# Kernel tuning notes

Measured on AMD Instinct MI355X. Metric: run time of the kernel, lower is better.

The kernel has to match this reference:

```python
import jax, jax.numpy as jnp
import numpy as np

B, N, D = 4, 8192, 128
H = 4 * D  # exp_factor * features
EPS = 1e-5


def layer_norm(x):
    # fresh nn.LayerNorm each call -> weight=1, bias=0 (no learned affine)
    mu = jnp.mean(x, axis=-1, keepdims=True)
    var = jnp.var(x, axis=-1, keepdims=True)
    return (x - mu) * jax.lax.rsqrt(var + EPS)


def setup_inputs() -> dict:
    key = jax.random.key(0)
    ks = jax.random.split(key, 8)
    x = jax.random.normal(ks[0], (B, N, D), dtype=jnp.float32)
    adj = jax.random.uniform(ks[1], (N, N), dtype=jnp.float32)
    attn_mask = jnp.ones((1,), dtype=jnp.int32)  # unused (torch masked_fill result discarded)
    pad_mask = jnp.ones((1,), dtype=jnp.int32)   # unused
    # FFN params (torch Linear default init scale ~ 1/sqrt(fan_in))
    w1 = jax.random.normal(ks[2], (D, H), dtype=jnp.float32) / np.sqrt(D)
    b1 = jnp.zeros((H,), dtype=jnp.float32)
    w2 = jax.random.normal(ks[3], (H, D), dtype=jnp.float32) / np.sqrt(H)
    b2 = jnp.zeros((D,), dtype=jnp.float32)
    return {"x": x, "adj": adj, "attn_mask": attn_mask, "pad_mask": pad_mask,
            "w1": w1, "b1": b1, "w2": w2, "b2": b2, "dim": 128}


def reference(x, adj, attn_mask, pad_mask, w1, b1, w2, b2, dim):
    # Sublayer 0: x + InrAwaSA(LN(x))
    h = layer_norm(x)                               # [B,N,D]
    # adj is provided -> scores = dense adj, shared across batch.
    # NOTE: masks are no-ops in the source (masked_fill not in-place).
    prob = jax.nn.softmax(adj, axis=-1)             # [N,N]
    attn_out = jnp.einsum('nm,bmd->bnd', prob, h)   # [B,N,D]
    x1 = x + attn_out
    # Sublayer 1: x1 + FFN(LN(x1))
    h1 = layer_norm(x1)
    ffn = jnp.maximum(h1 @ w1 + b1, 0.0) @ w2 + b2
    return x1 + ffn
```

## Files before the change

kernel.cpp:

```cpp
#include <hip/hip_runtime.h>
#include <hip/hip_bf16.h>

typedef __attribute__((ext_vector_type(8))) short bh8;
typedef __attribute__((ext_vector_type(4))) float fx4;

typedef const __attribute__((address_space(1))) unsigned int* gas_p;
typedef __attribute__((address_space(3))) unsigned int* las_p;

#define MFMA(a, b, c) __builtin_amdgcn_mfma_f32_16x16x32_bf16((a), (b), (c), 0, 0, 0)
#define MFMA8(a, b, c) __builtin_amdgcn_mfma_f32_16x16x32_fp8_fp8((a), (b), (c), 0, 0, 0)

__device__ __forceinline__ unsigned short f2bf(float f) {
  unsigned u = __builtin_bit_cast(unsigned, f);
  u += 0x7fff + ((u >> 16) & 1);
  return (unsigned short)(u >> 16);
}

__device__ __forceinline__ float bflo2f(unsigned u) { return __builtin_bit_cast(float, u << 16); }
__device__ __forceinline__ float bfhi2f(unsigned u) { return __builtin_bit_cast(float, u & 0xffff0000u); }

__device__ __forceinline__ void gld16(const void* g, void* l) {
  __builtin_amdgcn_global_load_lds((gas_p)g, (las_p)l, 16, 0, 0);
}

__global__ __launch_bounds__(256) void transpose_weights(const float* __restrict__ w1,
                                                         const float* __restrict__ w2,
                                                         unsigned short* __restrict__ w1t,
                                                         unsigned short* __restrict__ w2t) {
  const int tgl = blockIdx.x * 256 + threadIdx.x;
  { const int h = tgl >> 7, d = tgl & 127; w1t[tgl] = f2bf(w1[d * 512 + h]); }
  { const int d = tgl >> 9, h = tgl & 511; w2t[tgl] = f2bf(w2[h * 128 + d]); }
}

__global__ __launch_bounds__(256) void ln1_transpose(const float* __restrict__ x,
                                                     unsigned char* __restrict__ ht) {
  const int t = threadIdx.x, lane = t & 63, w = t >> 6;
  const int mt = blockIdx.x, b = blockIdx.y;
  __shared__ unsigned short tile[128 * 64];
  const float* xb = x + ((size_t)b * 8192 + (size_t)mt * 64) * 128;
  for (int it = 0; it < 16; ++it) {
    const int r = w * 16 + it;
    const float2 v = *(const float2*)(xb + r * 128 + lane * 2);
    float s = v.x + v.y, s2 = v.x * v.x + v.y * v.y;
    #pragma unroll
    for (int o = 1; o < 64; o <<= 1) { s += __shfl_xor(s, o); s2 += __shfl_xor(s2, o); }
    const float mean = s * 0.0078125f;
    const float var = s2 * 0.0078125f - mean * mean;
    const float rstd = rsqrtf(var + 1e-5f);
    const int mc = r >> 3, ml = r & 7;
    const int d0 = lane * 2, d1 = d0 + 1;
    tile[d0 * 64 + ((mc ^ (d0 & 7)) << 3) + ml] = f2bf((v.x - mean) * rstd);
    tile[d1 * 64 + ((mc ^ (d1 & 7)) << 3) + ml] = f2bf((v.y - mean) * rstd);
  }
  __syncthreads();
  unsigned char* hb = ht + (size_t)b * 128 * 8192 + (size_t)mt * 64;
  #pragma unroll
  for (int i = 0; i < 4; ++i) {
    const int idx = i * 256 + t;
    const int d = idx >> 3, mc = idx & 7;
    const bh8 vv = *(const bh8*)(tile + d * 64 + ((mc ^ (d & 7)) << 3));
    int lo = 0, hi = 0;
    lo = __builtin_amdgcn_cvt_pk_fp8_f32(bflo2f((unsigned short)vv[0]),
                                         bflo2f((unsigned short)vv[1]), lo, false);
    lo = __builtin_amdgcn_cvt_pk_fp8_f32(bflo2f((unsigned short)vv[2]),
                                         bflo2f((unsigned short)vv[3]), lo, true);
    hi = __builtin_amdgcn_cvt_pk_fp8_f32(bflo2f((unsigned short)vv[4]),
                                         bflo2f((unsigned short)vv[5]), hi, false);
    hi = __builtin_amdgcn_cvt_pk_fp8_f32(bflo2f((unsigned short)vv[6]),
                                         bflo2f((unsigned short)vv[7]), hi, true);
    *(uint2*)(hb + (size_t)d * 8192 + mc * 8) = (uint2){(unsigned)lo, (unsigned)hi};
  }
}

__global__ __launch_bounds__(256) void softmax_rows(const float* __restrict__ adj,
                                                    unsigned char* __restrict__ prob) {
  const int t = threadIdx.x, lane = t & 63, w = t >> 6;
  const size_t r = blockIdx.x;
  __shared__ float red[4];
  const fx4* row = (const fx4*)(adj + r * 8192);
  fx4 v[8];
  float lsum = 0.f;
  #pragma unroll
  for (int i = 0; i < 8; ++i) {
    const fx4 a = row[i * 256 + t];
    fx4 e;
    e.x = __expf(a.x);
    e.y = __expf(a.y);
    e.z = __expf(a.z);
    e.w = __expf(a.w);
    v[i] = e;
    lsum += e.x + e.y + e.z + e.w;
  }
  #pragma unroll
  for (int o = 1; o < 64; o <<= 1) lsum += __shfl_xor(lsum, o);
  if (lane == 0) red[w] = lsum;
  __syncthreads();
  const float rinv = 4096.f / (red[0] + red[1] + red[2] + red[3]);
  unsigned* po = (unsigned*)(prob + r * 8192);
  #pragma unroll
  for (int i = 0; i < 8; ++i) {
    int pk = 0;
    pk = __builtin_amdgcn_cvt_pk_fp8_f32(v[i].x * rinv, v[i].y * rinv, pk, false);
    pk = __builtin_amdgcn_cvt_pk_fp8_f32(v[i].z * rinv, v[i].w * rinv, pk, true);
    po[i * 256 + t] = (unsigned)pk;
  }
}

#define PH_SYNC { __builtin_amdgcn_sched_barrier(0); __builtin_amdgcn_s_barrier(); \
                  __builtin_amdgcn_sched_barrier(0); \
                  asm volatile("s_waitcnt lgkmcnt(0)" ::: "memory"); \
                  __builtin_amdgcn_sched_barrier(0); __builtin_amdgcn_s_setprio(1); }
#define PH_END  { __builtin_amdgcn_s_setprio(0); __builtin_amdgcn_sched_barrier(0); \
                  __builtin_amdgcn_s_barrier(); __builtin_amdgcn_sched_barrier(0); }
#define PH_END_VM2 { __builtin_amdgcn_s_setprio(0); \
                  asm volatile("s_waitcnt vmcnt(2)" ::: "memory"); \
                  __builtin_amdgcn_sched_barrier(0); __builtin_amdgcn_s_barrier(); \
                  __builtin_amdgcn_sched_barrier(0); }

__global__ __launch_bounds__(512, 2) void attn_gemm(const unsigned char* __restrict__ prob,
                                                    const unsigned char* __restrict__ ht,
                                                    unsigned short* __restrict__ pbuf) {
  const int t = threadIdx.x, lane = t & 63, w = t >> 6;
  const int wm = w >> 2, wn = w & 3;
  const int mt = blockIdx.x, nt = blockIdx.y, z = blockIdx.z;
  const int kbase = z * 2048;

  __shared__ unsigned char Al[2][2][128 * 64];
  __shared__ unsigned char Bl[2][2][128 * 64];

  fx4 acc[8][4];
  #pragma unroll
  for (int i = 0; i < 8; ++i)
    #pragma unroll
    for (int j = 0; j < 4; ++j) acc[i][j] = (fx4){0.f, 0.f, 0.f, 0.f};

  long afr[8], bf0[4], bf1[4];

  auto stageA = [&](int buf, int half, int tau) {
    const unsigned char* root = prob + (size_t)(mt * 256 + half * 128) * 8192 + kbase + tau * 64;
    const int r = t >> 2, c = t & 3;
    gld16(root + (size_t)r * 8192 + ((c ^ ((r >> 1) & 3)) << 4), &Al[buf][half][(t & ~63) * 16]);
  };
  auto stageB = [&](int buf, int half, int tau) {
    const unsigned char* root = ht + (size_t)(nt * 256 + half * 128) * 8192 + kbase + tau * 64;
    const int r = t >> 2, c = t & 3;
    gld16(root + (size_t)r * 8192 + ((c ^ ((r >> 1) & 3)) << 4), &Bl[buf][half][(t & ~63) * 16]);
  };
  auto ldA = [&](int buf, int mh) {
    #pragma unroll
    for (int mf = 0; mf < 4; ++mf)
      #pragma unroll
      for (int kk = 0; kk < 2; ++kk) {
        const int r = mh * 64 + mf * 16 + (lane & 15);
        const int sl = lane >> 4;
        const int g = kk * 2 + (sl >> 1), h = sl & 1;
        afr[mf * 2 + kk] =
            *(const long*)&Al[buf][wm][r * 64 + ((g ^ ((r >> 1) & 3)) << 4) + h * 8];
      }
  };
  auto ldB = [&](int buf, int nh, long* dst) {
    #pragma unroll
    for (int nf = 0; nf < 2; ++nf)
      #pragma unroll
      for (int kk = 0; kk < 2; ++kk) {
        const int c = (wn & 1) * 64 + nh * 32 + nf * 16 + (lane & 15);
        const int sl = lane >> 4;
        const int g = kk * 2 + (sl >> 1), h = sl & 1;
        dst[nf * 2 + kk] =
            *(const long*)&Bl[buf][wn >> 1][c * 64 + ((g ^ ((c >> 1) & 3)) << 4) + h * 8];
      }
  };
  auto mmq = [&](int mh, int nh, const long* bfr) {
    #pragma unroll
    for (int mf = 0; mf < 4; ++mf)
      #pragma unroll
      for (int nf = 0; nf < 2; ++nf)
        #pragma unroll
        for (int kk = 0; kk < 2; ++kk)
          acc[mh * 4 + mf][nh * 2 + nf] =
              MFMA8(afr[mf * 2 + kk], bfr[nf * 2 + kk], acc[mh * 4 + mf][nh * 2 + nf]);
  };

  stageA(0, 0, 0); stageA(0, 1, 0); stageB(0, 0, 0); stageB(0, 1, 0);
  stageB(1, 0, 1); stageB(1, 1, 1);
  asm volatile("s_waitcnt vmcnt(2)" ::: "memory");
  __builtin_amdgcn_sched_barrier(0);
  __builtin_amdgcn_s_barrier();
  __builtin_amdgcn_sched_barrier(0);

  for (int i = 0; i < 15; ++i) {
    const int t0 = 2 * i;
    ldA(0, 0); ldB(0, 0, bf0); stageA(1, 0, t0 + 1);
    PH_SYNC; mmq(0, 0, bf0); PH_END;
    ldB(0, 1, bf1); stageA(1, 1, t0 + 1);
    PH_SYNC; mmq(0, 1, bf1); PH_END;
    ldA(0, 1); stageB(0, 0, t0 + 2);
    PH_SYNC; mmq(1, 1, bf1); PH_END;
    stageB(0, 1, t0 + 2);
    PH_SYNC; mmq(1, 0, bf0); PH_END_VM2;
    ldA(1, 0); ldB(1, 0, bf0); stageA(0, 0, t0 + 2);
    PH_SYNC; mmq(0, 0, bf0); PH_END;
    ldB(1, 1, bf1); stageA(0, 1, t0 + 2);
    PH_SYNC; mmq(0, 1, bf1); PH_END;
    ldA(1, 1); stageB(1, 0, t0 + 3);
    PH_SYNC; mmq(1, 1, bf1); PH_END;
    stageB(1, 1, t0 + 3);
    PH_SYNC; mmq(1, 0, bf0); PH_END_VM2;
  }

  stageA(1, 0, 31); stageA(1, 1, 31);
  asm volatile("s_waitcnt vmcnt(0)" ::: "memory");
  __builtin_amdgcn_sched_barrier(0);
  __builtin_amdgcn_s_barrier();
  __builtin_amdgcn_sched_barrier(0);
  ldA(0, 0); ldB(0, 0, bf0); PH_SYNC; mmq(0, 0, bf0); PH_END;
  ldB(0, 1, bf1);            PH_SYNC; mmq(0, 1, bf1); PH_END;
  ldA(0, 1);                 PH_SYNC; mmq(1, 1, bf1); PH_END;
                             PH_SYNC; mmq(1, 0, bf0); PH_END;
  ldA(1, 0); ldB(1, 0, bf0); PH_SYNC; mmq(0, 0, bf0); PH_END;
  ldB(1, 1, bf1);            PH_SYNC; mmq(0, 1, bf1); PH_END;
  ldA(1, 1);                 PH_SYNC; mmq(1, 1, bf1); PH_END;
                             PH_SYNC; mmq(1, 0, bf0); PH_END;

  const float ds = 0.000244140625f;
  unsigned short* po = pbuf + (size_t)z * 8192 * 512;
  const int grow0 = mt * 256 + wm * 128;
  const int gcol0 = nt * 256 + (wn >> 1) * 128 + (wn & 1) * 64;
  #pragma unroll
  for (int mh = 0; mh < 2; ++mh)
    #pragma unroll
    for (int mf = 0; mf < 4; ++mf)
      #pragma unroll
      for (int nh = 0; nh < 2; ++nh)
        #pragma unroll
        for (int nf = 0; nf < 2; ++nf) {
          const int col = gcol0 + nh * 32 + nf * 16 + (lane & 15);
          #pragma unroll
          for (int q = 0; q < 4; ++q) {
            const int row = grow0 + mh * 64 + mf * 16 + (lane >> 4) * 4 + q;
            po[(size_t)row * 512 + col] = f2bf(acc[mh * 4 + mf][nh * 2 + nf][q] * ds);
          }
        }
}

#define SWZ16(ks, r) (((((ks) & 7) ^ ((r) & 7)) | ((ks) & 8)))
__global__ __launch_bounds__(512) void ln_ffn_kernel(const float* __restrict__ x,
                                                     const unsigned short* __restrict__ pbuf,
                                                     const unsigned short* __restrict__ w1t,
                                                     const unsigned short* __restrict__ w2t,
                                                     const float* __restrict__ b1,
                                                     const float* __restrict__ b2,
                                                     float* __restrict__ out) {
  const int t = threadIdx.x, lane = t & 63, w = t >> 6;
  const int wr = w >> 1, wc = w & 1;
  const int row0 = blockIdx.x * 128;
  __shared__ unsigned short As[128 * 128];
  __shared__ unsigned short W1c[128 * 128];
  __shared__ unsigned short W2c[128 * 128];
  __shared__ unsigned short Ts[128 * 128];

  auto stageW1 = [&](int hc) {
    #pragma unroll
    for (int i = 0; i < 4; ++i) {
      const int idx = i * 512 + t;
      const int row = idx >> 4, kc = idx & 15;
      const int kcs = (kc & 8) | ((kc & 7) ^ (row & 7));
      gld16(w1t + (size_t)(hc * 128 + row) * 128 + kcs * 8, W1c + (idx & ~63) * 8);
    }
  };
  auto stageW2 = [&](int hc) {
    #pragma unroll
    for (int i = 0; i < 4; ++i) {
      const int idx = i * 512 + t;
      const int row = idx >> 4, kc = idx & 15;
      const int kcs = (kc & 8) | ((kc & 7) ^ (row & 7));
      gld16(w2t + (size_t)row * 512 + hc * 128 + kcs * 8, W2c + (idx & ~63) * 8);
    }
  };

  stageW1(0); stageW2(0);

  const int r = t >> 2, q = t & 3, c0 = q * 32;
  const int rowg = row0 + r;
  const int bb = rowg >> 13, nn = rowg & 8191;
  float xv[32];
  {
    const float* xp = x + (size_t)rowg * 128 + c0;
    #pragma unroll
    for (int j = 0; j < 8; ++j) {
      const float4 v4 = *(const float4*)(xp + 4 * j);
      xv[4 * j] = v4.x; xv[4 * j + 1] = v4.y; xv[4 * j + 2] = v4.z; xv[4 * j + 3] = v4.w;
    }
    #pragma unroll
    for (int z = 0; z < 4; ++z) {
      const unsigned short* pp = pbuf + ((size_t)z * 8192 + nn) * 512 + bb * 128 + c0;
      #pragma unroll
      for (int j = 0; j < 4; ++j) {
        const bh8 pv = *(const bh8*)(pp + 8 * j);
        #pragma unroll
        for (int e = 0; e < 8; ++e) xv[8 * j + e] += bflo2f((unsigned short)pv[e]);
      }
    }
  }
  float s = 0.f, s2 = 0.f;
  #pragma unroll
  for (int j = 0; j < 32; ++j) { s += xv[j]; s2 += xv[j] * xv[j]; }
  s += __shfl_xor(s, 1); s2 += __shfl_xor(s2, 1);
  s += __shfl_xor(s, 2); s2 += __shfl_xor(s2, 2);
  const float mean = s * 0.0078125f;
  const float var = s2 * 0.0078125f - mean * mean;
  const float rstd = rsqrtf(var + 1e-5f);
  #pragma unroll
  for (int j = 0; j < 4; ++j) {
    const int g = q * 4 + j;
    bh8 pk;
    #pragma unroll
    for (int e = 0; e < 8; ++e) pk[e] = (short)f2bf((xv[8 * j + e] - mean) * rstd);
    *(bh8*)(As + r * 128 + SWZ16(g, r) * 8) = pk;
  }
  __syncthreads();

  fx4 accO[2][4];
  #pragma unroll
  for (int i = 0; i < 2; ++i)
    #pragma unroll
    for (int j = 0; j < 4; ++j) accO[i][j] = (fx4){0.f, 0.f, 0.f, 0.f};

  for (int hc = 0; hc < 4; ++hc) {
    if (hc > 0) stageW2(hc);
    fx4 accT[2][4];
    #pragma unroll
    for (int i = 0; i < 2; ++i)
      #pragma unroll
      for (int j = 0; j < 4; ++j) accT[i][j] = (fx4){0.f, 0.f, 0.f, 0.f};
    #pragma unroll
    for (int kk = 0; kk < 4; ++kk) {
      const int ks = kk * 4 + (lane >> 4);
      bh8 af[2], bfr[4];
      #pragma unroll
      for (int f = 0; f < 2; ++f) {
        const int ra = wr * 32 + f * 16 + (lane & 15);
        af[f] = *(const bh8*)(As + ra * 128 + SWZ16(ks, ra) * 8);
      }
      #pragma unroll
      for (int f = 0; f < 4; ++f) {
        const int rb = wc * 64 + f * 16 + (lane & 15);
        bfr[f] = *(const bh8*)(W1c + rb * 128 + SWZ16(ks, rb) * 8);
      }
      #pragma unroll
      for (int fm = 0; fm < 2; ++fm)
        #pragma unroll
        for (int fn = 0; fn < 4; ++fn) accT[fm][fn] = MFMA(af[fm], bfr[fn], accT[fm][fn]);
    }
    #pragma unroll
    for (int fm = 0; fm < 2; ++fm)
      #pragma unroll
      for (int fn = 0; fn < 4; ++fn) {
        const int col = wc * 64 + fn * 16 + (lane & 15);
        const float bv = b1[hc * 128 + col];
        const int c = col >> 3;
        #pragma unroll
        for (int qq = 0; qq < 4; ++qq) {
          const int row = wr * 32 + fm * 16 + (lane >> 4) * 4 + qq;
          float vv = accT[fm][fn][qq] + bv;
          vv = fmaxf(vv, 0.f);
          Ts[row * 128 + SWZ16(c, row) * 8 + (col & 7)] = f2bf(vv);
        }
      }
    __syncthreads();
    if (hc < 3) {
      stageW1(hc + 1);
    } else {
      float* dst = (r < 64) ? (float*)As + r * 128 + c0 : (float*)W1c + (r - 64) * 128 + c0;
      #pragma unroll
      for (int j = 0; j < 8; ++j)
        *(float4*)(dst + 4 * j) =
            (float4){xv[4 * j], xv[4 * j + 1], xv[4 * j + 2], xv[4 * j + 3]};
    }
    #pragma unroll
    for (int kk = 0; kk < 4; ++kk) {
      const int ks = kk * 4 + (lane >> 4);
      bh8 af[2], bfr[4];
      #pragma unroll
      for (int f = 0; f < 2; ++f) {
        const int ra = wr * 32 + f * 16 + (lane & 15);
        af[f] = *(const bh8*)(Ts + ra * 128 + SWZ16(ks, ra) * 8);
      }
      #pragma unroll
      for (int f = 0; f < 4; ++f) {
        const int rb = wc * 64 + f * 16 + (lane & 15);
        bfr[f] = *(const bh8*)(W2c + rb * 128 + SWZ16(ks, rb) * 8);
      }
      #pragma unroll
      for (int fm = 0; fm < 2; ++fm)
        #pragma unroll
        for (int fn = 0; fn < 4; ++fn) accO[fm][fn] = MFMA(af[fm], bfr[fn], accO[fm][fn]);
    }
    __syncthreads();
  }

  const float* x1a = (const float*)As;
  const float* x1b = (const float*)W1c;
  float* op = out + (size_t)row0 * 128;
  #pragma unroll
  for (int fm = 0; fm < 2; ++fm)
    #pragma unroll
    for (int fn = 0; fn < 4; ++fn) {
      const int col = wc * 64 + fn * 16 + (lane & 15);
      const float bv = b2[col];
      #pragma unroll
      for (int qq = 0; qq < 4; ++qq) {
        const int row = wr * 32 + fm * 16 + (lane >> 4) * 4 + qq;
        const float x1v = (row < 64) ? x1a[row * 128 + col] : x1b[(row - 64) * 128 + col];
        op[row * 128 + col] = x1v + accO[fm][fn][qq] + bv;
      }
    }
}

extern "C" void kernel_launch(void* const* d_in, const int* in_sizes, int n_in,
                              void* d_out, int out_size, void* d_ws, size_t ws_size,
                              hipStream_t stream) {
  const float* x   = (const float*)d_in[0];
  const float* adj = (const float*)d_in[1];
  const float* w1  = (const float*)d_in[4];
  const float* b1  = (const float*)d_in[5];
  const float* w2  = (const float*)d_in[6];
  const float* b2  = (const float*)d_in[7];
  float* out = (float*)d_out;

  char* p = (char*)d_ws;
  unsigned short* w1t  = (unsigned short*)p; p += (size_t)512 * 128 * 2;
  unsigned short* w2t  = (unsigned short*)p; p += (size_t)128 * 512 * 2;
  unsigned char*  ht   = (unsigned char*)p;  p += (size_t)4 * 128 * 8192;
  unsigned short* pbuf = (unsigned short*)p; p += (size_t)4 * 8192 * 512 * 2;
  unsigned char*  prob = (unsigned char*)p;  p += (size_t)8192 * 8192;

  transpose_weights<<<256, 256, 0, stream>>>(w1, w2, w1t, w2t);
  ln1_transpose<<<dim3(128, 4), 256, 0, stream>>>(x, ht);
  softmax_rows<<<8192, 256, 0, stream>>>(adj, prob);
  attn_gemm<<<dim3(32, 2, 4), 512, 0, stream>>>(prob, ht, pbuf);
  ln_ffn_kernel<<<256, 512, 0, stream>>>(x, pbuf, w1t, w2t, b1, b2, out);
}
```

Measured before the change: 181.7 us.

## Switch attention GEMM to scaled 16x16x128 FP8 MFMA with deeper K tiles

Replaces the 16x16x32 fp8 MFMA with the gfx950 scaled f8f6f4 16x16x128 MFMA, using unit scales (0x7f exponent bias). K tile per stage doubles from 64 to 128 bytes, so shared-memory buffers double, the swizzle changes to an 8-way XOR on 16-byte groups, and each thread issues two async global-to-LDS loads per stage. The loop runs half as many iterations, with vmcnt thresholds raised to match. The aim is fewer MFMA issues and higher matrix throughput per instruction. In exchange, LDS use grows to 128 KB, which may limit occupancy to one block per CU despite the launch bound of 2.

```diff
diff --git a/kernel.cpp b/kernel.cpp
--- a/kernel.cpp
+++ b/kernel.cpp
@@ -3,12 +3,15 @@
 
 typedef __attribute__((ext_vector_type(8))) short bh8;
 typedef __attribute__((ext_vector_type(4))) float fx4;
+typedef __attribute__((ext_vector_type(8))) int i32x8;
+typedef __attribute__((ext_vector_type(4))) int i32x4;
 
 typedef const __attribute__((address_space(1))) unsigned int* gas_p;
 typedef __attribute__((address_space(3))) unsigned int* las_p;
 
 #define MFMA(a, b, c) __builtin_amdgcn_mfma_f32_16x16x32_bf16((a), (b), (c), 0, 0, 0)
-#define MFMA8(a, b, c) __builtin_amdgcn_mfma_f32_16x16x32_fp8_fp8((a), (b), (c), 0, 0, 0)
+#define MFMAS(a, b, c) __builtin_amdgcn_mfma_scale_f32_16x16x128_f8f6f4( \
+    (a), (b), (c), 0, 0, 0, 0x7f7f7f7f, 0, 0x7f7f7f7f)
 
 __device__ __forceinline__ unsigned short f2bf(float f) {
   unsigned u = __builtin_bit_cast(unsigned, f);
@@ -17,7 +20,6 @@
 }
 
 __device__ __forceinline__ float bflo2f(unsigned u) { return __builtin_bit_cast(float, u << 16); }
-__device__ __forceinline__ float bfhi2f(unsigned u) { return __builtin_bit_cast(float, u & 0xffff0000u); }
 
 __device__ __forceinline__ void gld16(const void* g, void* l) {
   __builtin_amdgcn_global_load_lds((gas_p)g, (las_p)l, 16, 0, 0);
@@ -112,8 +114,8 @@
                   __builtin_amdgcn_sched_barrier(0); __builtin_amdgcn_s_setprio(1); }
 #define PH_END  { __builtin_amdgcn_s_setprio(0); __builtin_amdgcn_sched_barrier(0); \
                   __builtin_amdgcn_s_barrier(); __builtin_amdgcn_sched_barrier(0); }
-#define PH_END_VM2 { __builtin_amdgcn_s_setprio(0); \
-                  asm volatile("s_waitcnt vmcnt(2)" ::: "memory"); \
+#define PH_END_VM4 { __builtin_amdgcn_s_setprio(0); \
+                  asm volatile("s_waitcnt vmcnt(4)" ::: "memory"); \
                   __builtin_amdgcn_sched_barrier(0); __builtin_amdgcn_s_barrier(); \
                   __builtin_amdgcn_sched_barrier(0); }
 
@@ -125,8 +127,8 @@
   const int mt = blockIdx.x, nt = blockIdx.y, z = blockIdx.z;
   const int kbase = z * 2048;
 
-  __shared__ unsigned char Al[2][2][128 * 64];
-  __shared__ unsigned char Bl[2][2][128 * 64];
+  __shared__ unsigned char Al[2][2][128 * 128];
+  __shared__ unsigned char Bl[2][2][128 * 128];
 
   fx4 acc[8][4];
   #pragma unroll
@@ -134,61 +136,64 @@
     #pragma unroll
     for (int j = 0; j < 4; ++j) acc[i][j] = (fx4){0.f, 0.f, 0.f, 0.f};
 
-  long afr[8], bf0[4], bf1[4];
+  i32x8 afr[4], bf0[2], bf1[2];
 
   auto stageA = [&](int buf, int half, int tau) {
-    const unsigned char* root = prob + (size_t)(mt * 256 + half * 128) * 8192 + kbase + tau * 64;
-    const int r = t >> 2, c = t & 3;
-    gld16(root + (size_t)r * 8192 + ((c ^ ((r >> 1) & 3)) << 4), &Al[buf][half][(t & ~63) * 16]);
+    const unsigned char* root = prob + (size_t)(mt * 256 + half * 128) * 8192 + kbase + tau * 128;
+    #pragma unroll
+    for (int j = 0; j < 2; ++j) {
+      const int idx = j * 512 + t;
+      const int r = idx >> 3, g = idx & 7;
+      gld16(root + (size_t)r * 8192 + ((g ^ (r & 7)) << 4), &Al[buf][half][idx * 16]);
+    }
   };
   auto stageB = [&](int buf, int half, int tau) {
-    const unsigned char* root = ht + (size_t)(nt * 256 + half * 128) * 8192 + kbase + tau * 64;
-    const int r = t >> 2, c = t & 3;
-    gld16(root + (size_t)r * 8192 + ((c ^ ((r >> 1) & 3)) << 4), &Bl[buf][half][(t & ~63) * 16]);
+    const unsigned char* root = ht + (size_t)(nt * 256 + half * 128) * 8192 + kbase + tau * 128;
+    #pragma unroll
+    for (int j = 0; j < 2; ++j) {
+      const int idx = j * 512 + t;
+      const int r = idx >> 3, g = idx & 7;
+      gld16(root + (size_t)r * 8192 + ((g ^ (r & 7)) << 4), &Bl[buf][half][idx * 16]);
+    }
   };
   auto ldA = [&](int buf, int mh) {
     #pragma unroll
+    for (int mf = 0; mf < 4; ++mf) {
+      const int r = mh * 64 + mf * 16 + (lane & 15);
+      const int gb = (lane >> 4) * 2;
+      const unsigned char* base = &Al[buf][wm][r * 128];
+      const i32x4 lo = *(const i32x4*)(base + ((gb ^ (r & 7)) << 4));
+      const i32x4 hi = *(const i32x4*)(base + (((gb + 1) ^ (r & 7)) << 4));
+      afr[mf] = (i32x8){lo.x, lo.y, lo.z, lo.w, hi.x, hi.y, hi.z, hi.w};
+    }
+  };
+  auto ldB = [&](int buf, int nh, i32x8* dst) {
+    #pragma unroll
+    for (int nf = 0; nf < 2; ++nf) {
+      const int c = (wn & 1) * 64 + nh * 32 + nf * 16 + (lane & 15);
+      const int gb = (lane >> 4) * 2;
+      const unsigned char* base = &Bl[buf][wn >> 1][c * 128];
+      const i32x4 lo = *(const i32x4*)(base + ((gb ^ (c & 7)) << 4));
+      const i32x4 hi = *(const i32x4*)(base + (((gb + 1) ^ (c & 7)) << 4));
+      dst[nf] = (i32x8){lo.x, lo.y, lo.z, lo.w, hi.x, hi.y, hi.z, hi.w};
+    }
+  };
+  auto mmq = [&](int mh, int nh, const i32x8* bfr) {
+    #pragma unroll
     for (int mf = 0; mf < 4; ++mf)
       #pragma unroll
-      for (int kk = 0; kk < 2; ++kk) {
-        const int r = mh * 64 + mf * 16 + (lane & 15);
-        const int sl = lane >> 4;
-        const int g = kk * 2 + (sl >> 1), h = sl & 1;
-        afr[mf * 2 + kk] =
-            *(const long*)&Al[buf][wm][r * 64 + ((g ^ ((r >> 1) & 3)) << 4) + h * 8];
-      }
-  };
-  auto ldB = [&](int buf, int nh, long* dst) {
-    #pragma unroll
-    for (int nf = 0; nf < 2; ++nf)
-      #pragma unroll
-      for (int kk = 0; kk < 2; ++kk) {
-        const int c = (wn & 1) * 64 + nh * 32 + nf * 16 + (lane & 15);
-        const int sl = lane >> 4;
-        const int g = kk * 2 + (sl >> 1), h = sl & 1;
-        dst[nf * 2 + kk] =
-            *(const long*)&Bl[buf][wn >> 1][c * 64 + ((g ^ ((c >> 1) & 3)) << 4) + h * 8];
-      }
-  };
-  auto mmq = [&](int mh, int nh, const long* bfr) {
-    #pragma unroll
-    for (int mf = 0; mf < 4; ++mf)
-      #pragma unroll
       for (int nf = 0; nf < 2; ++nf)
-        #pragma unroll
-        for (int kk = 0; kk < 2; ++kk)
-          acc[mh * 4 + mf][nh * 2 + nf] =
-              MFMA8(afr[mf * 2 + kk], bfr[nf * 2 + kk], acc[mh * 4 + mf][nh * 2 + nf]);
+        acc[mh * 4 + mf][nh * 2 + nf] = MFMAS(afr[mf], bfr[nf], acc[mh * 4 + mf][nh * 2 + nf]);
   };
 
   stageA(0, 0, 0); stageA(0, 1, 0); stageB(0, 0, 0); stageB(0, 1, 0);
   stageB(1, 0, 1); stageB(1, 1, 1);
-  asm volatile("s_waitcnt vmcnt(2)" ::: "memory");
+  asm volatile("s_waitcnt vmcnt(4)" ::: "memory");
   __builtin_amdgcn_sched_barrier(0);
   __builtin_amdgcn_s_barrier();
   __builtin_amdgcn_sched_barrier(0);
 
-  for (int i = 0; i < 15; ++i) {
+  for (int i = 0; i < 7; ++i) {
     const int t0 = 2 * i;
     ldA(0, 0); ldB(0, 0, bf0); stageA(1, 0, t0 + 1);
     PH_SYNC; mmq(0, 0, bf0); PH_END;
@@ -197,7 +202,7 @@
     ldA(0, 1); stageB(0, 0, t0 + 2);
     PH_SYNC; mmq(1, 1, bf1); PH_END;
     stageB(0, 1, t0 + 2);
-    PH_SYNC; mmq(1, 0, bf0); PH_END_VM2;
+    PH_SYNC; mmq(1, 0, bf0); PH_END_VM4;
     ldA(1, 0); ldB(1, 0, bf0); stageA(0, 0, t0 + 2);
     PH_SYNC; mmq(0, 0, bf0); PH_END;
     ldB(1, 1, bf1); stageA(0, 1, t0 + 2);
@@ -205,10 +210,10 @@
     ldA(1, 1); stageB(1, 0, t0 + 3);
     PH_SYNC; mmq(1, 1, bf1); PH_END;
     stageB(1, 1, t0 + 3);
-    PH_SYNC; mmq(1, 0, bf0); PH_END_VM2;
-  }
-
-  stageA(1, 0, 31); stageA(1, 1, 31);
+    PH_SYNC; mmq(1, 0, bf0); PH_END_VM4;
+  }
+
+  stageA(1, 0, 15); stageA(1, 1, 15);
   asm volatile("s_waitcnt vmcnt(0)" ::: "memory");
   __builtin_amdgcn_sched_barrier(0);
   __builtin_amdgcn_s_barrier();
```

Measured after the change: 157.6 us. 1.15x faster.
